# Kernel optimization log

Hardware: AMD Instinct MI355X
Metric: run time of the kernel (lower is better)

## Reference

```python
import jax, jax.numpy as jnp
import numpy as np

B, T, HE, L, HD = 512, 512, 512, 64, 512

def setup_inputs() -> dict:
    key = jax.random.key(0)
    ks = jax.random.split(key, 16)
    def w(k, shape):
        return jax.random.normal(k, shape, dtype=jnp.float32) * 0.05
    z32 = lambda n: jnp.zeros((n,), jnp.float32)
    return {
        "input_tensor": jax.random.normal(ks[0], (B, T, 1), dtype=jnp.float32),
        # encoder LSTMCell (keras gate order i, f, g, o)
        "enc_W": w(ks[1], (1, 4 * HE)),
        "enc_U": w(ks[2], (HE, 4 * HE)),
        "enc_b": z32(4 * HE),
        # encoder mu / std heads
        "emu_W": w(ks[3], (HE, L)), "emu_b": z32(L),
        "estd_W": w(ks[4], (HE, L)), "estd_b": z32(L),
        # decoder first-state dense (tanh)
        "dfs_W": w(ks[5], (L, HD)), "dfs_b": z32(HD),
        # decoder LSTMCell
        "dec_W": w(ks[6], (L, 4 * HD)),
        "dec_U": w(ks[7], (HD, 4 * HD)),
        "dec_b": z32(4 * HD),
        # decoder mu / std heads (Dense(1))
        "dmu_W": w(ks[8], (HD, 1)), "dmu_b": z32(1),
        "dstd_W": w(ks[9], (HD, 1)), "dstd_b": z32(1),
    }

def _lstm_update(gates, c):
    i, f, g, o = jnp.split(gates, 4, axis=-1)
    c_new = jax.nn.sigmoid(f) * c + jax.nn.sigmoid(i) * jnp.tanh(g)
    h_new = jax.nn.sigmoid(o) * jnp.tanh(c_new)
    return h_new, c_new

def reference(input_tensor, enc_W, enc_U, enc_b, emu_W, emu_b, estd_W, estd_b,
              dfs_W, dfs_b, dec_W, dec_U, dec_b, dmu_W, dmu_b, dstd_W, dstd_b):
    x = input_tensor
    Bn, Tn = x.shape[0], x.shape[1]
    He = enc_U.shape[0]

    # ---- encoder: LSTM over time, keep final h ----
    def enc_step(carry, xt):
        h, c = carry
        gates = xt @ enc_W + h @ enc_U + enc_b
        return _lstm_update(gates, c), None
    h0 = jnp.zeros((Bn, He), x.dtype)
    (hT, _), _ = jax.lax.scan(enc_step, (h0, h0), jnp.swapaxes(x, 0, 1))

    mu_enc = hT @ emu_W + emu_b                       # [B, L]
    sigma_enc = jax.nn.softplus(hT @ estd_W + estd_b)  # [B, L]
    z = mu_enc  # call() uses reparam=False -> latent returns mu

    # ---- decoder: LSTM fed constant z each step ----
    hd = jnp.tanh(z @ dfs_W + dfs_b)                  # [B, HD]
    cd = jnp.zeros_like(hd)
    zin = z @ dec_W + dec_b                           # input projection constant over t
    def dec_step(carry, _):
        h, c = carry
        h_new, c_new = _lstm_update(zin + h @ dec_U, c)
        mu = h_new @ dmu_W + dmu_b                    # [B, 1]
        sg = h_new @ dstd_W + dstd_b
        return (h_new, c_new), (mu, sg)
    _, (mus, sgs) = jax.lax.scan(dec_step, (hd, cd), None, length=Tn)

    mu_dec = jnp.swapaxes(mus, 0, 1)                  # [B, T, 1]
    sigma_dec = jax.nn.softplus(jnp.swapaxes(sgs, 0, 1))
    return (mu_dec, sigma_dec, mu_enc, sigma_enc)
```

## Files before the change

kernel.cpp:

```cpp
#include <hip/hip_runtime.h>


#define B_   512
#define T_   512
#define H_   512
#define NGR  32
#define WPG  8
#define RPG  16
#define UPW  64

typedef _Float16 f16;
typedef _Float16 f16x8 __attribute__((ext_vector_type(8)));
typedef _Float16 f16x4 __attribute__((ext_vector_type(4)));
typedef float f32x16 __attribute__((ext_vector_type(16)));
typedef unsigned long long u64;

#define OFF_SG_DEC 262144
#define OFF_MU_ENC 524288
#define OFF_SG_ENC 557056

__device__ __forceinline__ float sigm_(float x) { return 1.f / (1.f + __expf(-x)); }
__device__ __forceinline__ float tanh_(float x) {
  float t = fabsf(x);
  float e = __expf(2.f * t);
  float r = 1.f - 2.f / (e + 1.f);
  return x < 0.f ? -r : r;
}
__device__ __forceinline__ float softplus_(float x) {
  return fmaxf(x, 0.f) + log1pf(__expf(-fabsf(x)));
}

__global__ void pack_U(const float* __restrict__ U, f16* __restrict__ Upk) {
  const int e = blockIdx.x * 256 + threadIdx.x;
  const int j = e & 7, lane = (e >> 3) & 63, ks = (e >> 9) & 31;
  const int w = (e >> 14) & 7, wg = (e >> 17) & 7;
  const int ccol = lane & 31, khalf = lane >> 5;
  const int uu = ccol >> 2, gate = ccol & 3;
  const int k = ks * 16 + khalf * 8 + j;
  const int gcol = gate * 512 + wg * UPW + w * 8 + uu;
  Upk[e] = (f16)U[k * 2048 + gcol];
}

template <int IS_DEC>
__global__ void __launch_bounds__(512, 1)
lstm_rec(const f16* __restrict__ Upk,
         const float* __restrict__ xin,
         const float* __restrict__ gw,
         const float* __restrict__ gb,
         f16* __restrict__ hbuf,
         float* __restrict__ accmu,
         float* __restrict__ accsg,
         int* __restrict__ flags) {
  const int bid = blockIdx.x;
  const int wg = (bid >> 3) & 7;
  const int g = (bid & 7) * 4 + (bid >> 6);
  const int tid = threadIdx.x;
  const int wave = tid >> 6, lane = tid & 63;
  const int R0 = g * RPG;
  const int U0 = wg * UPW;

  const int ccol = lane & 31, khalf = lane >> 5;
  f16x8 Breg[32];
#pragma unroll
  for (int ks = 0; ks < 32; ++ks) {
    const f16* p = Upk + (((wg * 8 + wave) * 32 + ks) << 9) + lane * 8;
    asm volatile("global_load_dwordx4 %0, %1, off\n\ts_waitcnt vmcnt(0)"
                 : "=v"(Breg[ks]) : "v"(p));
  }

  const int row = tid >> 4;
  const int q = (tid & 15) * 4;
  float addv[16], xw[16], dmur[4], dstdr[4];
  if (tid < 256) {
#pragma unroll
    for (int m = 0; m < 4; ++m) {
#pragma unroll
      for (int gt = 0; gt < 4; ++gt) {
        const int col = gt * 512 + U0 + q + m;
        if (IS_DEC) {
          addv[m * 4 + gt] = xin[(R0 + row) * 2048 + col];
          xw[m * 4 + gt] = 0.f;
        } else {
          addv[m * 4 + gt] = gb[col];
          xw[m * 4 + gt] = gw[col];
        }
      }
      if (IS_DEC) {
        dmur[m] = gw[U0 + q + m];
        dstdr[m] = gb[U0 + q + m];
      } else {
        dmur[m] = 0.f;
        dstdr[m] = 0.f;
      }
    }
  }

  float cst[4] = {0.f, 0.f, 0.f, 0.f};

  __shared__ __align__(16) f16 hstage[RPG * 536];
  __shared__ float gatesLds[RPG * 260];
  __shared__ float pmuLds[RPG * 17];
  __shared__ float psgLds[RPG * 17];

  const int hrow = lane & 15;
  int* const myflag = &flags[(g * WPG + wg) * 32];
  int* const grpflags = &flags[(g * WPG) * 32];

  for (int t = 0; t < T_; ++t) {
    const u64* hsrc64 = (const u64*)(hbuf + (t & 1) * (B_ * H_) + R0 * H_);
    float xv = 0.f;
    if (!IS_DEC && tid < 256) xv = xin[(R0 + row) * T_ + t];
#pragma unroll
    for (int i = 0; i < 4; ++i) {
      const int w = tid + i * 512;
      const int r = w >> 7, c8 = w & 127;
      u64 v = __hip_atomic_load(hsrc64 + w, __ATOMIC_RELAXED,
                                __HIP_MEMORY_SCOPE_AGENT);
      *(u64*)&hstage[r * 536 + c8 * 4] = v;
    }
    __syncthreads();

    f32x16 acc;
#pragma unroll
    for (int j = 0; j < 16; ++j) acc[j] = 0.f;
#pragma unroll
    for (int ks = 0; ks < 32; ++ks) {
      f16x8 a = *(const f16x8*)&hstage[hrow * 536 + ks * 16 + khalf * 8];
      acc = __builtin_amdgcn_mfma_f32_32x32x16_f16(a, Breg[ks], acc, 0, 0, 0);
    }
#pragma unroll
    for (int r = 0; r < 8; ++r) {
      const int orow = (r & 3) + 8 * (r >> 2) + 4 * khalf;
      gatesLds[orow * 260 + wave * 32 + ccol] = acc[r];
    }
    __syncthreads();

    union { f16x4 h4; u64 u; } cv;
    if (tid < 256) {
      float hn[4];
#pragma unroll
      for (int m = 0; m < 4; ++m) {
        float ga[4];
#pragma unroll
        for (int gt = 0; gt < 4; ++gt) {
          float v = gatesLds[row * 260 + (q + m) * 4 + gt] + addv[m * 4 + gt];
          if (!IS_DEC) v += xv * xw[m * 4 + gt];
          ga[gt] = v;
        }
        const float iv = sigm_(ga[0]);
        const float fv = sigm_(ga[1]);
        const float gv = tanh_(ga[2]);
        const float ov = sigm_(ga[3]);
        const float cn = fv * cst[m] + iv * gv;
        cst[m] = cn;
        hn[m] = ov * tanh_(cn);
      }
#pragma unroll
      for (int m = 0; m < 4; ++m) cv.h4[m] = (f16)hn[m];
      f16* hdst = hbuf + ((t + 1) & 1) * (B_ * H_) + (R0 + row) * H_ + U0 + q;
      __hip_atomic_store((u64*)hdst, cv.u, __ATOMIC_RELAXED,
                         __HIP_MEMORY_SCOPE_AGENT);
      if (IS_DEC) {
        float pmu = 0.f, psg = 0.f;
#pragma unroll
        for (int m = 0; m < 4; ++m) {
          pmu += (float)cv.h4[m] * dmur[m];
          psg += (float)cv.h4[m] * dstdr[m];
        }
        pmuLds[row * 17 + (tid & 15)] = pmu;
        psgLds[row * 17 + (tid & 15)] = psg;
      }
    }

    asm volatile("s_waitcnt vmcnt(0)" ::: "memory");
    __syncthreads();
    if (t + 1 < T_ && tid == 0)
      __hip_atomic_store(myflag, t + 1, __ATOMIC_RELAXED,
                         __HIP_MEMORY_SCOPE_AGENT);

    if (IS_DEC) {
      if (tid < RPG) {
        float s = 0.f;
#pragma unroll
        for (int j = 0; j < 16; ++j) s += pmuLds[tid * 17 + j];
        unsafeAtomicAdd(&accmu[(R0 + tid) * T_ + t], s);
      } else if (tid < 2 * RPG) {
        const int rr = tid - RPG;
        float s = 0.f;
#pragma unroll
        for (int j = 0; j < 16; ++j) s += psgLds[rr * 17 + j];
        unsafeAtomicAdd(&accsg[(R0 + rr) * T_ + t], s);
      }
    }

    if (t + 1 < T_) {
      if (tid < WPG) {
        while (__hip_atomic_load(&grpflags[tid * 32], __ATOMIC_RELAXED,
                                 __HIP_MEMORY_SCOPE_AGENT) < t + 1) {
          asm volatile("s_sleep 1");
        }
      }
      __syncthreads();
    }
  }
}

__global__ void enc_heads(const f16* __restrict__ h0, const float* __restrict__ emuW,
                          const float* __restrict__ emub, const float* __restrict__ estdW,
                          const float* __restrict__ estdb, float* __restrict__ out,
                          float* __restrict__ z) {
  const int b = blockIdx.x, tid = threadIdx.x;
  __shared__ float hrow[512];
  for (int k = tid; k < 512; k += 128)
    hrow[k] = (float)h0[b * H_ + k];
  __syncthreads();
  const int head = tid >> 6, l = tid & 63;
  const float* W = head ? estdW : emuW;
  float a = 0.f;
#pragma unroll 8
  for (int k = 0; k < 512; ++k) a += hrow[k] * W[k * 64 + l];
  if (head == 0) {
    const float v = a + emub[l];
    out[OFF_MU_ENC + b * 64 + l] = v;
    z[b * 64 + l] = v;
  } else {
    out[OFF_SG_ENC + b * 64 + l] = softplus_(a + estdb[l]);
  }
}

__global__ void dec_prep(const float* __restrict__ z, const float* __restrict__ dfsW,
                         const float* __restrict__ dfsb, const float* __restrict__ decW,
                         const float* __restrict__ decb, f16* __restrict__ hbuf,
                         float* __restrict__ zin) {
  const int b = blockIdx.x, tid = threadIdx.x;
  __shared__ float zl[64];
  if (tid < 64) zl[tid] = z[b * 64 + tid];
  __syncthreads();
  for (int c = tid; c < 512; c += 256) {
    float a = dfsb[c];
#pragma unroll
    for (int l = 0; l < 64; ++l) a += zl[l] * dfsW[l * 512 + c];
    hbuf[b * H_ + c] = (f16)tanh_(a);
  }
  for (int c = tid; c < 2048; c += 256) {
    float a = decb[c];
#pragma unroll
    for (int l = 0; l < 64; ++l) a += zl[l] * decW[l * 2048 + c];
    zin[b * 2048 + c] = a;
  }
}

__global__ void finalize_k(const float* __restrict__ accmu, const float* __restrict__ accsg,
                           const float* __restrict__ dmub, const float* __restrict__ dstdb,
                           float* __restrict__ out) {
  const int i = blockIdx.x * 256 + threadIdx.x;
  out[i] = accmu[i] + dmub[0];
  out[OFF_SG_DEC + i] = softplus_(accsg[i] + dstdb[0]);
}

extern "C" void kernel_launch(void* const* d_in, const int* in_sizes, int n_in,
                              void* d_out, int out_size, void* d_ws, size_t ws_size,
                              hipStream_t stream) {
  (void)in_sizes; (void)n_in; (void)out_size; (void)ws_size;
  const float* x     = (const float*)d_in[0];
  const float* encW  = (const float*)d_in[1];
  const float* encU  = (const float*)d_in[2];
  const float* encb  = (const float*)d_in[3];
  const float* emuW  = (const float*)d_in[4];
  const float* emub  = (const float*)d_in[5];
  const float* estdW = (const float*)d_in[6];
  const float* estdb = (const float*)d_in[7];
  const float* dfsW  = (const float*)d_in[8];
  const float* dfsb  = (const float*)d_in[9];
  const float* decW  = (const float*)d_in[10];
  const float* decU  = (const float*)d_in[11];
  const float* decb  = (const float*)d_in[12];
  const float* dmuW  = (const float*)d_in[13];
  const float* dmub  = (const float*)d_in[14];
  const float* dstdW = (const float*)d_in[15];
  const float* dstdb = (const float*)d_in[16];

  char* ws = (char*)d_ws;
  f16* hbuf    = (f16*)(ws + 0);
  float* accmu = (float*)(ws + (1u << 20));
  float* accsg = (float*)(ws + (2u << 20));
  int* flags   = (int*)(ws + (3u << 20));
  f16* UpkE    = (f16*)(ws + (3u << 20) + 65536);
  float* zin   = (float*)(ws + (3u << 20) + 65536);
  f16* UpkD    = (f16*)(ws + (7u << 20) + 65536);
  float* z     = (float*)(ws + (9u << 20) + 65536);
  float* out   = (float*)d_out;

  hipMemsetAsync(d_ws, 0, (3u << 20) + 65536, stream);

  hipLaunchKernelGGL(pack_U, dim3(8192), dim3(256), 0, stream, encU, UpkE);
  hipLaunchKernelGGL(pack_U, dim3(8192), dim3(256), 0, stream, decU, UpkD);

  hipLaunchKernelGGL((lstm_rec<0>), dim3(256), dim3(512), 0, stream,
                     UpkE, x, encW, encb, hbuf, (float*)nullptr, (float*)nullptr,
                     flags);
  hipLaunchKernelGGL(enc_heads, dim3(512), dim3(128), 0, stream,
                     hbuf, emuW, emub, estdW, estdb, out, z);
  hipLaunchKernelGGL(dec_prep, dim3(512), dim3(256), 0, stream,
                     z, dfsW, dfsb, decW, decb, hbuf, zin);
  hipLaunchKernelGGL((lstm_rec<1>), dim3(256), dim3(512), 0, stream,
                     UpkD, zin, dmuW, dstdW, hbuf, accmu, accsg, flags + 8192);
  hipLaunchKernelGGL(finalize_k, dim3(1024), dim3(256), 0, stream,
                     accmu, accsg, dmub, dstdb, out);
}
```

Before: 4.237 ms.

## Replace flag barriers with generation-tagged hidden-state words and split rows into two halves

Each hidden value is now stored as a 32-bit word holding a 16-bit step tag next to the fp16 value. Consumers spin on the data itself until it carries the current tag, so the per-workgroup flag stores, s_waitcnt drain and group flag polling are gone. Each block's 16 rows are split into two 8-row halves, and loading half B overlaps the MFMA and gate math of half A. This doubles hidden-state traffic and halves the MFMA row use per 32x32 tile. It also moves the decoder head reduction to wave shuffles.

```diff
diff --git a/kernel.cpp b/kernel.cpp
--- a/kernel.cpp
+++ b/kernel.cpp
@@ -1,19 +1,15 @@
 #include <hip/hip_runtime.h>
 
 
-#define B_   512
-#define T_   512
-#define H_   512
-#define NGR  32
-#define WPG  8
-#define RPG  16
-#define UPW  64
+#define B_ 512
+#define T_ 512
+#define H_ 512
 
 typedef _Float16 f16;
 typedef _Float16 f16x8 __attribute__((ext_vector_type(8)));
-typedef _Float16 f16x4 __attribute__((ext_vector_type(4)));
 typedef float f32x16 __attribute__((ext_vector_type(16)));
 typedef unsigned long long u64;
+typedef unsigned int u32;
 
 #define OFF_SG_DEC 262144
 #define OFF_MU_ENC 524288
@@ -28,6 +24,12 @@
 }
 __device__ __forceinline__ float softplus_(float x) {
   return fmaxf(x, 0.f) + log1pf(__expf(-fabsf(x)));
+}
+__device__ __forceinline__ int fresh_(u64 w, u32 g) {
+  return ((u32)(w >> 48) == g) & (((u32)(w >> 16) & 0xffffu) == g);
+}
+__device__ __forceinline__ u32 packh_(u64 w) {
+  return (u32)(w & 0xffffu) | (((u32)(w >> 32) & 0xffffu) << 16);
 }
 
 __global__ void pack_U(const float* __restrict__ U, f16* __restrict__ Upk) {
@@ -37,7 +39,7 @@
   const int ccol = lane & 31, khalf = lane >> 5;
   const int uu = ccol >> 2, gate = ccol & 3;
   const int k = ks * 16 + khalf * 8 + j;
-  const int gcol = gate * 512 + wg * UPW + w * 8 + uu;
+  const int gcol = gate * 512 + wg * 64 + w * 8 + uu;
   Upk[e] = (f16)U[k * 2048 + gcol];
 }
 
@@ -45,21 +47,21 @@
 __global__ void __launch_bounds__(512, 1)
 lstm_rec(const f16* __restrict__ Upk,
          const float* __restrict__ xin,
-         const float* __restrict__ gw,
-         const float* __restrict__ gb,
-         f16* __restrict__ hbuf,
+         const float* __restrict__ wa,
+         const float* __restrict__ wb,
+         u32* __restrict__ hbuf,
          float* __restrict__ accmu,
-         float* __restrict__ accsg,
-         int* __restrict__ flags) {
+         float* __restrict__ accsg) {
   const int bid = blockIdx.x;
-  const int wg = (bid >> 3) & 7;
-  const int g = (bid & 7) * 4 + (bid >> 6);
-  const int tid = threadIdx.x;
-  const int wave = tid >> 6, lane = tid & 63;
-  const int R0 = g * RPG;
-  const int U0 = wg * UPW;
-
+  const int s = bid >> 3;
+  const int j = (bid & 7) * 4 + (s & 3);
+  const int wg = s >> 2;
+  const int tid = threadIdx.x, wave = tid >> 6, lane = tid & 63;
+  const int U0 = wg * 64;
+  const int RA = j * 16, RB = j * 16 + 8;
+  const u32 GB = IS_DEC ? 0x8000u : 0u;
   const int ccol = lane & 31, khalf = lane >> 5;
+
   f16x8 Breg[32];
 #pragma unroll
   for (int ks = 0; ks < 32; ++ks) {
@@ -68,151 +70,200 @@
                  : "=v"(Breg[ks]) : "v"(p));
   }
 
-  const int row = tid >> 4;
-  const int q = (tid & 15) * 4;
-  float addv[16], xw[16], dmur[4], dstdr[4];
-  if (tid < 256) {
-#pragma unroll
-    for (int m = 0; m < 4; ++m) {
-#pragma unroll
-      for (int gt = 0; gt < 4; ++gt) {
-        const int col = gt * 512 + U0 + q + m;
-        if (IS_DEC) {
-          addv[m * 4 + gt] = xin[(R0 + row) * 2048 + col];
-          xw[m * 4 + gt] = 0.f;
-        } else {
-          addv[m * 4 + gt] = gb[col];
-          xw[m * 4 + gt] = gw[col];
-        }
-      }
+  const int erow = tid >> 6, eu = tid & 63;
+  float xwv[4], bias[4], addA[4], addB[4];
+  float dmu_w = 0.f, dstd_w = 0.f;
+#pragma unroll
+  for (int gt = 0; gt < 4; ++gt) {
+    const int col = gt * 512 + U0 + eu;
+    if (IS_DEC) {
+      addA[gt] = xin[(RA + erow) * 2048 + col];
+      addB[gt] = xin[(RB + erow) * 2048 + col];
+      xwv[gt] = 0.f; bias[gt] = 0.f;
+    } else {
+      bias[gt] = wb[col];
+      xwv[gt] = wa[col];
+      addA[gt] = 0.f; addB[gt] = 0.f;
+    }
+  }
+  if (IS_DEC) { dmu_w = wa[U0 + eu]; dstd_w = wb[U0 + eu]; }
+
+  float cA = 0.f, cB = 0.f;
+
+  __shared__ __align__(16) f16 bufA[8 * 520];
+  __shared__ __align__(16) f16 bufB[8 * 520];
+  __shared__ __align__(16) float gatesL[8 * 264];
+
+  int lrow[4], lcol[4], gidxA[4], gidxB[4];
+#pragma unroll
+  for (int i = 0; i < 4; ++i) {
+    const int w = tid + i * 512;
+    lrow[i] = w >> 8; lcol[i] = w & 255;
+    gidxA[i] = (RA + lrow[i]) * 256 + lcol[i];
+    gidxB[i] = (RB + lrow[i]) * 256 + lcol[i];
+  }
+  const u64* hb64 = (const u64*)hbuf;
+
+  u64 wAr[4], wBr[4];
+#pragma unroll
+  for (int i = 0; i < 4; ++i)
+    wAr[i] = __hip_atomic_load(hb64 + gidxA[i], __ATOMIC_RELAXED,
+                               __HIP_MEMORY_SCOPE_AGENT);
+  asm volatile("" ::: "memory");
+
+  for (int t = 0; t < T_; ++t) {
+    const int b0 = (t & 1) * 131072;
+    const int b1 = ((t + 1) & 1) * 131072;
+    const int c1 = ((t + 1) & 1) * 262144;
+    const u32 gr = GB + (u32)t, gn = GB + (u32)t + 1u;
+
+    while (!(fresh_(wAr[0], gr) & fresh_(wAr[1], gr) &
+             fresh_(wAr[2], gr) & fresh_(wAr[3], gr))) {
+#pragma unroll
+      for (int i = 0; i < 4; ++i)
+        wAr[i] = __hip_atomic_load(hb64 + b0 + gidxA[i], __ATOMIC_RELAXED,
+                                   __HIP_MEMORY_SCOPE_AGENT);
+    }
+#pragma unroll
+    for (int i = 0; i < 4; ++i)
+      *(u32*)&bufA[lrow[i] * 520 + lcol[i] * 2] = packh_(wAr[i]);
+    __syncthreads();
+
+#pragma unroll
+    for (int i = 0; i < 4; ++i)
+      wBr[i] = __hip_atomic_load(hb64 + b0 + gidxB[i], __ATOMIC_RELAXED,
+                                 __HIP_MEMORY_SCOPE_AGENT);
+    asm volatile("" ::: "memory");
+
+    {
+      f32x16 acc;
+#pragma unroll
+      for (int q = 0; q < 16; ++q) acc[q] = 0.f;
+#pragma unroll
+      for (int ks = 0; ks < 32; ++ks) {
+        f16x8 a = *(const f16x8*)&bufA[(lane & 7) * 520 + ks * 16 + khalf * 8];
+        acc = __builtin_amdgcn_mfma_f32_32x32x16_f16(a, Breg[ks], acc, 0, 0, 0);
+      }
+#pragma unroll
+      for (int r = 0; r < 4; ++r)
+        gatesL[(r + 4 * khalf) * 264 + wave * 32 + ccol] = acc[r];
+    }
+    __syncthreads();
+
+    {
+      const float4 g4 = *(const float4*)&gatesL[erow * 264 + (eu >> 3) * 32 + (eu & 7) * 4];
+      float ga0, ga1, ga2, ga3;
       if (IS_DEC) {
-        dmur[m] = gw[U0 + q + m];
-        dstdr[m] = gb[U0 + q + m];
+        ga0 = g4.x + addA[0]; ga1 = g4.y + addA[1];
+        ga2 = g4.z + addA[2]; ga3 = g4.w + addA[3];
       } else {
-        dmur[m] = 0.f;
-        dstdr[m] = 0.f;
-      }
-    }
-  }
-
-  float cst[4] = {0.f, 0.f, 0.f, 0.f};
-
-  __shared__ __align__(16) f16 hstage[RPG * 536];
-  __shared__ float gatesLds[RPG * 260];
-  __shared__ float pmuLds[RPG * 17];
-  __shared__ float psgLds[RPG * 17];
-
-  const int hrow = lane & 15;
-  int* const myflag = &flags[(g * WPG + wg) * 32];
-  int* const grpflags = &flags[(g * WPG) * 32];
-
-  for (int t = 0; t < T_; ++t) {
-    const u64* hsrc64 = (const u64*)(hbuf + (t & 1) * (B_ * H_) + R0 * H_);
-    float xv = 0.f;
-    if (!IS_DEC && tid < 256) xv = xin[(R0 + row) * T_ + t];
-#pragma unroll
-    for (int i = 0; i < 4; ++i) {
-      const int w = tid + i * 512;
-      const int r = w >> 7, c8 = w & 127;
-      u64 v = __hip_atomic_load(hsrc64 + w, __ATOMIC_RELAXED,
-                                __HIP_MEMORY_SCOPE_AGENT);
-      *(u64*)&hstage[r * 536 + c8 * 4] = v;
-    }
-    __syncthreads();
-
-    f32x16 acc;
-#pragma unroll
-    for (int j = 0; j < 16; ++j) acc[j] = 0.f;
-#pragma unroll
-    for (int ks = 0; ks < 32; ++ks) {
-      f16x8 a = *(const f16x8*)&hstage[hrow * 536 + ks * 16 + khalf * 8];
-      acc = __builtin_amdgcn_mfma_f32_32x32x16_f16(a, Breg[ks], acc, 0, 0, 0);
-    }
-#pragma unroll
-    for (int r = 0; r < 8; ++r) {
-      const int orow = (r & 3) + 8 * (r >> 2) + 4 * khalf;
-      gatesLds[orow * 260 + wave * 32 + ccol] = acc[r];
-    }
-    __syncthreads();
-
-    union { f16x4 h4; u64 u; } cv;
-    if (tid < 256) {
-      float hn[4];
-#pragma unroll
-      for (int m = 0; m < 4; ++m) {
-        float ga[4];
-#pragma unroll
-        for (int gt = 0; gt < 4; ++gt) {
-          float v = gatesLds[row * 260 + (q + m) * 4 + gt] + addv[m * 4 + gt];
-          if (!IS_DEC) v += xv * xw[m * 4 + gt];
-          ga[gt] = v;
-        }
-        const float iv = sigm_(ga[0]);
-        const float fv = sigm_(ga[1]);
-        const float gv = tanh_(ga[2]);
-        const float ov = sigm_(ga[3]);
-        const float cn = fv * cst[m] + iv * gv;
-        cst[m] = cn;
-        hn[m] = ov * tanh_(cn);
-      }
-#pragma unroll
-      for (int m = 0; m < 4; ++m) cv.h4[m] = (f16)hn[m];
-      f16* hdst = hbuf + ((t + 1) & 1) * (B_ * H_) + (R0 + row) * H_ + U0 + q;
-      __hip_atomic_store((u64*)hdst, cv.u, __ATOMIC_RELAXED,
+        const float xv = xin[(RA + erow) * T_ + t];
+        ga0 = g4.x + bias[0] + xv * xwv[0];
+        ga1 = g4.y + bias[1] + xv * xwv[1];
+        ga2 = g4.z + bias[2] + xv * xwv[2];
+        ga3 = g4.w + bias[3] + xv * xwv[3];
+      }
+      const float cn = sigm_(ga1) * cA + sigm_(ga0) * tanh_(ga2);
+      cA = cn;
+      const float hn = sigm_(ga3) * tanh_(cn);
+      union { f16 h; unsigned short u; } hc; hc.h = (f16)hn;
+      __hip_atomic_store(hbuf + c1 + (RA + erow) * 512 + U0 + eu,
+                         (gn << 16) | (u32)hc.u, __ATOMIC_RELAXED,
                          __HIP_MEMORY_SCOPE_AGENT);
       if (IS_DEC) {
-        float pmu = 0.f, psg = 0.f;
-#pragma unroll
-        for (int m = 0; m < 4; ++m) {
-          pmu += (float)cv.h4[m] * dmur[m];
-          psg += (float)cv.h4[m] * dstdr[m];
+        float smu = hn * dmu_w, ssg = hn * dstd_w;
+#pragma unroll
+        for (int o = 32; o; o >>= 1) {
+          smu += __shfl_xor(smu, o);
+          ssg += __shfl_xor(ssg, o);
         }
-        pmuLds[row * 17 + (tid & 15)] = pmu;
-        psgLds[row * 17 + (tid & 15)] = psg;
-      }
-    }
-
-    asm volatile("s_waitcnt vmcnt(0)" ::: "memory");
+        if (lane == 0) {
+          unsafeAtomicAdd(&accmu[(RA + erow) * T_ + t], smu);
+          unsafeAtomicAdd(&accsg[(RA + erow) * T_ + t], ssg);
+        }
+      }
+    }
+
+    while (!(fresh_(wBr[0], gr) & fresh_(wBr[1], gr) &
+             fresh_(wBr[2], gr) & fresh_(wBr[3], gr))) {
+#pragma unroll
+      for (int i = 0; i < 4; ++i)
+        wBr[i] = __hip_atomic_load(hb64 + b0 + gidxB[i], __ATOMIC_RELAXED,
+                                   __HIP_MEMORY_SCOPE_AGENT);
+    }
+#pragma unroll
+    for (int i = 0; i < 4; ++i)
+      *(u32*)&bufB[lrow[i] * 520 + lcol[i] * 2] = packh_(wBr[i]);
     __syncthreads();
-    if (t + 1 < T_ && tid == 0)
-      __hip_atomic_store(myflag, t + 1, __ATOMIC_RELAXED,
+
+#pragma unroll
+    for (int i = 0; i < 4; ++i)
+      wAr[i] = __hip_atomic_load(hb64 + b1 + gidxA[i], __ATOMIC_RELAXED,
+                                 __HIP_MEMORY_SCOPE_AGENT);
+    asm volatile("" ::: "memory");
+
+    {
+      f32x16 acc;
+#pragma unroll
+      for (int q = 0; q < 16; ++q) acc[q] = 0.f;
+#pragma unroll
+      for (int ks = 0; ks < 32; ++ks) {
+        f16x8 a = *(const f16x8*)&bufB[(lane & 7) * 520 + ks * 16 + khalf * 8];
+        acc = __builtin_amdgcn_mfma_f32_32x32x16_f16(a, Breg[ks], acc, 0, 0, 0);
+      }
+#pragma unroll
+      for (int r = 0; r < 4; ++r)
+        gatesL[(r + 4 * khalf) * 264 + wave * 32 + ccol] = acc[r];
+    }
+    __syncthreads();
+
+    {
+      const float4 g4 = *(const float4*)&gatesL[erow * 264 + (eu >> 3) * 32 + (eu & 7) * 4];
+      float ga0, ga1, ga2, ga3;
+      if (IS_DEC) {
+        ga0 = g4.x + addB[0]; ga1 = g4.y + addB[1];
+        ga2 = g4.z + addB[2]; ga3 = g4.w + addB[3];
+      } else {
+        const float xv = xin[(RB + erow) * T_ + t];
+        ga0 = g4.x + bias[0] + xv * xwv[0];
+        ga1 = g4.y + bias[1] + xv * xwv[1];
+        ga2 = g4.z + bias[2] + xv * xwv[2];
+        ga3 = g4.w + bias[3] + xv * xwv[3];
+      }
+      const float cn = sigm_(ga1) * cB + sigm_(ga0) * tanh_(ga2);
+      cB = cn;
+      const float hn = sigm_(ga3) * tanh_(cn);
+      union { f16 h; unsigned short u; } hc; hc.h = (f16)hn;
+      __hip_atomic_store(hbuf + c1 + (RB + erow) * 512 + U0 + eu,
+                         (gn << 16) | (u32)hc.u, __ATOMIC_RELAXED,
                          __HIP_MEMORY_SCOPE_AGENT);
-
-    if (IS_DEC) {
-      if (tid < RPG) {
-        float s = 0.f;
-#pragma unroll
-        for (int j = 0; j < 16; ++j) s += pmuLds[tid * 17 + j];
-        unsafeAtomicAdd(&accmu[(R0 + tid) * T_ + t], s);
-      } else if (tid < 2 * RPG) {
-        const int rr = tid - RPG;
-        float s = 0.f;
-#pragma unroll
-        for (int j = 0; j < 16; ++j) s += psgLds[rr * 17 + j];
-        unsafeAtomicAdd(&accsg[(R0 + rr) * T_ + t], s);
-      }
-    }
-
-    if (t + 1 < T_) {
-      if (tid < WPG) {
-        while (__hip_atomic_load(&grpflags[tid * 32], __ATOMIC_RELAXED,
-                                 __HIP_MEMORY_SCOPE_AGENT) < t + 1) {
-          asm volatile("s_sleep 1");
+      if (IS_DEC) {
+        float smu = hn * dmu_w, ssg = hn * dstd_w;
+#pragma unroll
+        for (int o = 32; o; o >>= 1) {
+          smu += __shfl_xor(smu, o);
+          ssg += __shfl_xor(ssg, o);
         }
-      }
-      __syncthreads();
-    }
-  }
-}
-
-__global__ void enc_heads(const f16* __restrict__ h0, const float* __restrict__ emuW,
+        if (lane == 0) {
+          unsafeAtomicAdd(&accmu[(RB + erow) * T_ + t], smu);
+          unsafeAtomicAdd(&accsg[(RB + erow) * T_ + t], ssg);
+        }
+      }
+    }
+  }
+}
+
+__global__ void enc_heads(const u32* __restrict__ h0, const float* __restrict__ emuW,
                           const float* __restrict__ emub, const float* __restrict__ estdW,
                           const float* __restrict__ estdb, float* __restrict__ out,
                           float* __restrict__ z) {
   const int b = blockIdx.x, tid = threadIdx.x;
   __shared__ float hrow[512];
-  for (int k = tid; k < 512; k += 128)
-    hrow[k] = (float)h0[b * H_ + k];
+  for (int k = tid; k < 512; k += 128) {
+    union { unsigned short u; f16 h; } c;
+    c.u = (unsigned short)(h0[b * 512 + k] & 0xffffu);
+    hrow[k] = (float)c.h;
+  }
   __syncthreads();
   const int head = tid >> 6, l = tid & 63;
   const float* W = head ? estdW : emuW;
@@ -230,7 +281,7 @@
 
 __global__ void dec_prep(const float* __restrict__ z, const float* __restrict__ dfsW,
                          const float* __restrict__ dfsb, const float* __restrict__ decW,
-                         const float* __restrict__ decb, f16* __restrict__ hbuf,
+                         const float* __restrict__ decb, u32* __restrict__ hbuf,
                          float* __restrict__ zin) {
   const int b = blockIdx.x, tid = threadIdx.x;
   __shared__ float zl[64];
@@ -240,7 +291,8 @@
     float a = dfsb[c];
 #pragma unroll
     for (int l = 0; l < 64; ++l) a += zl[l] * dfsW[l * 512 + c];
-    hbuf[b * H_ + c] = (f16)tanh_(a);
+    union { f16 h; unsigned short u; } hc; hc.h = (f16)tanh_(a);
+    hbuf[b * 512 + c] = (0x8000u << 16) | (u32)hc.u;
   }
   for (int c = tid; c < 2048; c += 256) {
     float a = decb[c];
@@ -281,30 +333,28 @@
   const float* dstdb = (const float*)d_in[16];
 
   char* ws = (char*)d_ws;
-  f16* hbuf    = (f16*)(ws + 0);
-  float* accmu = (float*)(ws + (1u << 20));
-  float* accsg = (float*)(ws + (2u << 20));
-  int* flags   = (int*)(ws + (3u << 20));
-  f16* UpkE    = (f16*)(ws + (3u << 20) + 65536);
-  float* zin   = (float*)(ws + (3u << 20) + 65536);
-  f16* UpkD    = (f16*)(ws + (7u << 20) + 65536);
-  float* z     = (float*)(ws + (9u << 20) + 65536);
+  u32*   hbuf  = (u32*)(ws + 0);
+  float* accmu = (float*)(ws + (2u << 20));
+  float* accsg = (float*)(ws + (3u << 20));
+  f16*   UpkE  = (f16*)(ws + (4u << 20));
+  float* zin   = (float*)(ws + (4u << 20));
+  f16*   UpkD  = (f16*)(ws + (8u << 20));
+  float* z     = (float*)(ws + (10u << 20));
   float* out   = (float*)d_out;
 
-  hipMemsetAsync(d_ws, 0, (3u << 20) + 65536, stream);
-
-  hipLaunchKernelGGL(pack_U, dim3(8192), dim3(256), 0, stream, encU, UpkE);
-  hipLaunchKernelGGL(pack_U, dim3(8192), dim3(256), 0, stream, decU, UpkD);
+  hipMemsetAsync(d_ws, 0, 4u << 20, stream);
+
+  hipLaunchKernelGGL(pack_U, dim3(4096), dim3(256), 0, stream, encU, UpkE);
+  hipLaunchKernelGGL(pack_U, dim3(4096), dim3(256), 0, stream, decU, UpkD);
 
   hipLaunchKernelGGL((lstm_rec<0>), dim3(256), dim3(512), 0, stream,
-                     UpkE, x, encW, encb, hbuf, (float*)nullptr, (float*)nullptr,
-                     flags);
+                     UpkE, x, encW, encb, hbuf, (float*)nullptr, (float*)nullptr);
   hipLaunchKernelGGL(enc_heads, dim3(512), dim3(128), 0, stream,
                      hbuf, emuW, emub, estdW, estdb, out, z);
   hipLaunchKernelGGL(dec_prep, dim3(512), dim3(256), 0, stream,
                      z, dfsW, dfsb, decW, decb, hbuf, zin);
   hipLaunchKernelGGL((lstm_rec<1>), dim3(256), dim3(512), 0, stream,
-                     UpkD, zin, dmuW, dstdW, hbuf, accmu, accsg, flags + 8192);
+                     UpkD, zin, dmuW, dstdW, hbuf, accmu, accsg);
   hipLaunchKernelGGL(finalize_k, dim3(1024), dim3(256), 0, stream,
                      accmu, accsg, dmub, dstdb, out);
 }
```

After: 4.916 ms. +16.0%, slower.
